# Optimization experiments

Measured on AMD Instinct MI355X. Metric: run time of the kernel, lower is better.

The kernel has to match this reference:

```python
import jax, jax.numpy as jnp
import numpy as np

B, S, E, H, D = 64, 512, 512, 8, 64  # batch, n_steps, embedding_size, head_count, QKV_dim

def setup_inputs() -> dict:
    key = jax.random.key(0)
    ks = jax.random.split(key, 7)
    x = jax.random.normal(ks[0], (B, S, E), dtype=jnp.float32)
    mask = jax.random.randint(ks[1], (B, S), 0, 2).astype(jnp.float32)  # 1 = masked out
    WQ = jax.random.normal(ks[2], (H, E, D), dtype=jnp.float32) * 0.1
    WK = jax.random.normal(ks[3], (H, E, D), dtype=jnp.float32) * 0.1
    WV = jax.random.normal(ks[4], (H, E, D), dtype=jnp.float32) * 0.1
    BE = jax.random.normal(ks[5], (S, E), dtype=jnp.float32) * 0.1
    WO = jax.random.normal(ks[6], (H * D, E), dtype=jnp.float32) * 0.1
    return {"x": x, "mask": mask, "WQ": WQ, "WK": WK, "WV": WV, "BE": BE, "WO": WO}

def reference(x, mask, WQ, WK, WV, BE, WO):
    # add learned positional bias
    h = x + BE  # [B,S,E]
    # per-head projections, vectorized over heads
    Q = jnp.einsum('bse,hed->bhsd', h, WQ)
    K = jnp.einsum('bse,hed->bhsd', h, WK)
    V = jnp.einsum('bse,hed->bhsd', h, WV)
    # NOTE: original scales by sqrt(embedding_size), not sqrt(QKV_dim)
    scores = jnp.einsum('bhsd,bhtd->bhst', Q, K) / np.sqrt(E).astype(np.float32)
    # additive mask trick: mask tiled over query dim, key positions masked where mask==1
    scores = scores - mask[:, None, None, :] * 1e10
    alpha = jax.nn.softmax(scores, axis=-1)  # [B,H,S,S]
    attn = jnp.einsum('bhst,bhtd->bhsd', alpha, V)  # [B,H,S,D]
    # concat heads along feature dim -> [B,S,H*D], then output projection
    attn = jnp.transpose(attn, (0, 2, 1, 3)).reshape(x.shape[0], x.shape[1], -1)
    return attn @ WO  # [B,S,E]
```

## Files before the change

### kernel.cpp

```cpp
#include <hip/hip_runtime.h>
#include <hip/hip_bf16.h>


#define Bn 64
#define Sn 512
#define En 512
#define Hn 8
#define Dn 64

typedef __attribute__((ext_vector_type(8))) short s8v;
typedef __attribute__((ext_vector_type(4))) float f4v;

__device__ __forceinline__ unsigned short f2bf(float f) {
    union { float f; unsigned int u; } v; v.f = f;
    unsigned int u = v.u;
    u += 0x7fffu + ((u >> 16) & 1u);
    return (unsigned short)(u >> 16);
}

__device__ __forceinline__ void async16(const unsigned short* g, unsigned short* l) {
    __builtin_amdgcn_global_load_lds((const __attribute__((address_space(1))) void*)g,
                                     (__attribute__((address_space(3))) void*)l, 16, 0, 0);
}
__device__ __forceinline__ void async4(const float* g, float* l) {
    __builtin_amdgcn_global_load_lds((const __attribute__((address_space(1))) void*)g,
                                     (__attribute__((address_space(3))) void*)l, 4, 0, 0);
}

__global__ __launch_bounds__(256) void prep_all(const float* __restrict__ x,
                                                const float* __restrict__ BE,
                                                const float* __restrict__ WQ,
                                                const float* __restrict__ WK,
                                                const float* __restrict__ WV,
                                                const float* __restrict__ WO,
                                                unsigned short* __restrict__ hbf,
                                                unsigned short* __restrict__ Wqkvt,
                                                unsigned short* __restrict__ WOt) {
    int bid = blockIdx.x;
    if (bid < 16384) {
        int i = (bid * 256 + threadIdx.x) * 4;
        int se = i % (Sn * En);
        float4 a = *(const float4*)(x + i);
        float4 b = *(const float4*)(BE + se);
        ushort4 o;
        o.x = f2bf(a.x + b.x); o.y = f2bf(a.y + b.y);
        o.z = f2bf(a.z + b.z); o.w = f2bf(a.w + b.w);
        *(ushort4*)(hbf + i) = o;
    } else {
        int idx = (bid - 16384) * 256 + threadIdx.x;
        const int NW = 3 * Hn * Dn * En;
        if (idx < NW) {
            int e = idx & 511;
            int d = (idx >> 9) & 63;
            int h = (idx >> 15) & 7;
            int m = idx >> 18;
            const float* W = (m == 0) ? WQ : (m == 1) ? WK : WV;
            Wqkvt[idx] = f2bf(W[(h * En + e) * Dn + d]);
        } else {
            int j = idx - NW;
            int n = j & 511;
            int e = j >> 9;
            WOt[j] = f2bf(WO[n * En + e]);
        }
    }
}

__device__ __forceinline__ void mfma8(const s8v& a0k0, const s8v& a0k1,
                                      const s8v& a1k0, const s8v& a1k1,
                                      f4v* acc0, f4v* acc1,
                                      const s8v (&bq)[4][2], bool sw) {
    if (sw) {
#pragma unroll
        for (int n = 0; n < 4; n++) {
            acc0[n] = __builtin_amdgcn_mfma_f32_16x16x32_bf16(bq[n][0], a0k0, acc0[n], 0, 0, 0);
            acc0[n] = __builtin_amdgcn_mfma_f32_16x16x32_bf16(bq[n][1], a0k1, acc0[n], 0, 0, 0);
            acc1[n] = __builtin_amdgcn_mfma_f32_16x16x32_bf16(bq[n][0], a1k0, acc1[n], 0, 0, 0);
            acc1[n] = __builtin_amdgcn_mfma_f32_16x16x32_bf16(bq[n][1], a1k1, acc1[n], 0, 0, 0);
        }
    } else {
#pragma unroll
        for (int n = 0; n < 4; n++) {
            acc0[n] = __builtin_amdgcn_mfma_f32_16x16x32_bf16(a0k0, bq[n][0], acc0[n], 0, 0, 0);
            acc0[n] = __builtin_amdgcn_mfma_f32_16x16x32_bf16(a0k1, bq[n][1], acc0[n], 0, 0, 0);
            acc1[n] = __builtin_amdgcn_mfma_f32_16x16x32_bf16(a1k0, bq[n][0], acc1[n], 0, 0, 0);
            acc1[n] = __builtin_amdgcn_mfma_f32_16x16x32_bf16(a1k1, bq[n][1], acc1[n], 0, 0, 0);
        }
    }
}

__global__ __launch_bounds__(512, 2) void qkv_gemm(const unsigned short* __restrict__ hbf,
                                                   const unsigned short* __restrict__ Wqkvt,
                                                   unsigned short* __restrict__ Qo,
                                                   unsigned short* __restrict__ Ko,
                                                   unsigned short* __restrict__ Vt) {
    __shared__ __align__(16) unsigned short As[2][16384];
    __shared__ __align__(16) unsigned short Bs[2][16384];

    int lin = blockIdx.y * 6 + blockIdx.x;
    int swz = (lin & 7) * 96 + (lin >> 3);
    int mb = swz / 6, nbv = swz - mb * 6;

    int tid = threadIdx.x;
    int w = tid >> 6, lane = tid & 63, quad = lane >> 4, l16 = lane & 15, l7 = l16 & 7;
    int wr = w >> 2, wcn = w & 3;

    const unsigned short* Ag = hbf + (size_t)mb * 256 * 512;
    const unsigned short* Bg = Wqkvt + (size_t)nbv * 256 * 512;

    int colbase = nbv * 256 + wcn * 64;
    bool swapQK = colbase < 1024;

    int ha = (lane >> 3) & 1;
    int ca = w * 4 + (lane >> 4);
    int aG0 = (ca + 128 * ha) * 512 + ((lane & 7) ^ (ca & 7)) * 8;
    int rb0 = w * 8 + (lane >> 3);
    int bG0 = rb0 * 512 + ((lane & 7) ^ (rb0 & 7)) * 8;

    int arow = 2 * l16 + wr;
    int aseg0 = (quad ^ l7) * 8;
    int aseg1 = ((4 + quad) ^ l7) * 8;

    f4v acc[8][4];
#pragma unroll
    for (int i = 0; i < 8; i++)
#pragma unroll
        for (int n = 0; n < 4; n++) acc[i][n] = (f4v){0.f, 0.f, 0.f, 0.f};
    s8v bq[4][2];

#define STA8(o_, p_, kt_) async16(Ag + aG0 + (p_) * 16384 + (kt_) * 64, &As[o_][(p_) * 4096 + w * 512])
#define STB8(o_, q_, kt_) async16(Bg + bG0 + (q_) * 32768 + (kt_) * 64, &Bs[o_][(q_) * 4096 + w * 512])

#define PHASE8(P, STAGES, GATE)                                                   \
    do {                                                                          \
        if ((P) == 0) {                                                           \
            _Pragma("unroll")                                                     \
            for (int n = 0; n < 4; n++) {                                         \
                int br = (wcn * 64 + n * 16 + l16) * 64;                          \
                bq[n][0] = *(const s8v*)&Bs_s[br + aseg0];                        \
                bq[n][1] = *(const s8v*)&Bs_s[br + aseg1];                        \
            }                                                                     \
        }                                                                         \
        s8v a0k0 = *(const s8v*)&As_s[(((P) * 2 + 0) * 32 + arow) * 64 + aseg0];  \
        s8v a0k1 = *(const s8v*)&As_s[(((P) * 2 + 0) * 32 + arow) * 64 + aseg1];  \
        s8v a1k0 = *(const s8v*)&As_s[(((P) * 2 + 1) * 32 + arow) * 64 + aseg0];  \
        s8v a1k1 = *(const s8v*)&As_s[(((P) * 2 + 1) * 32 + arow) * 64 + aseg1];  \
        STAGES;                                                                   \
        __builtin_amdgcn_s_barrier();                                             \
        asm volatile("s_waitcnt lgkmcnt(0)" ::: "memory");                        \
        __builtin_amdgcn_s_setprio(1);                                            \
        mfma8(a0k0, a0k1, a1k0, a1k1, &acc[(P) * 2][0], &acc[(P) * 2 + 1][0], bq, swapQK); \
        __builtin_amdgcn_s_setprio(0);                                            \
        GATE;                                                                     \
        __builtin_amdgcn_s_barrier();                                             \
    } while (0)

    STB8(0, 0, 0); STB8(0, 1, 0); STB8(0, 2, 0); STB8(0, 3, 0);
    STA8(0, 0, 0); STA8(0, 1, 0); STA8(0, 2, 0); STA8(0, 3, 0);
    asm volatile("s_waitcnt vmcnt(0)" ::: "memory");
    __builtin_amdgcn_s_barrier();

    for (int k = 0; k < 7; k++) {
        int s = k & 1, o = s ^ 1, kt = k + 1;
        const unsigned short* As_s = &As[s][0];
        const unsigned short* Bs_s = &Bs[s][0];
        PHASE8(0, { STB8(o, 0, kt); STB8(o, 1, kt); STA8(o, 0, kt); },
               asm volatile("s_waitcnt vmcnt(6)" ::: "memory"));
        PHASE8(1, { STB8(o, 2, kt); STA8(o, 1, kt); },
               asm volatile("s_waitcnt vmcnt(6)" ::: "memory"));
        PHASE8(2, { STB8(o, 3, kt); STA8(o, 2, kt); },
               asm volatile("s_waitcnt vmcnt(7)" ::: "memory"));
        PHASE8(3, { STA8(o, 3, kt); },
               asm volatile("s_waitcnt vmcnt(2)" ::: "memory"));
    }
    {
        const unsigned short* As_s = &As[1][0];
        const unsigned short* Bs_s = &Bs[1][0];
        PHASE8(0, {}, asm volatile("s_waitcnt vmcnt(3)" ::: "memory"));
        PHASE8(1, {}, asm volatile("s_waitcnt vmcnt(1)" ::: "memory"));
        PHASE8(2, {}, asm volatile("s_waitcnt vmcnt(0)" ::: "memory"));
        PHASE8(3, {}, (void)0);
    }
#undef PHASE8
#undef STA8
#undef STB8

    int mat = colbase >> 9;
    int h = (colbase >> 6) & 7;
    int b_idx = mb >> 1;
    const float qscale = 0.06375873f;

    if (swapQK) {
        unsigned short* op = (mat == 0) ? Qo : Ko;
        float sc = (mat == 0) ? qscale : 1.0f;
#pragma unroll
        for (int mi = 0; mi < 8; mi++)
#pragma unroll
            for (int n = 0; n < 4; n++) {
                int s_ = (mb & 1) * 256 + wr * 128 + mi * 16 + l16;
                int d0 = n * 16 + quad * 4;
                ushort4 pk;
                pk.x = f2bf(acc[mi][n][0] * sc);
                pk.y = f2bf(acc[mi][n][1] * sc);
                pk.z = f2bf(acc[mi][n][2] * sc);
                pk.w = f2bf(acc[mi][n][3] * sc);
                *(ushort4*)&op[(size_t)((b_idx * Hn + h) * Sn + s_) * Dn + d0] = pk;
            }
    } else {
#pragma unroll
        for (int mi = 0; mi < 8; mi++)
#pragma unroll
            for (int n = 0; n < 4; n++) {
                int d = n * 16 + l16;
                int srow = (mb & 1) * 256 + wr * 128 + mi * 16 + quad * 4;
                ushort4 pk;
                pk.x = f2bf(acc[mi][n][0]); pk.y = f2bf(acc[mi][n][1]);
                pk.z = f2bf(acc[mi][n][2]); pk.w = f2bf(acc[mi][n][3]);
                *(ushort4*)&Vt[(size_t)((b_idx * Hn + h) * Dn + d) * Sn + srow] = pk;
            }
    }
}

__global__ __launch_bounds__(512) void attn_kernel(const unsigned short* __restrict__ Q,
                                                   const unsigned short* __restrict__ K,
                                                   const unsigned short* __restrict__ Vt,
                                                   const float* __restrict__ mask,
                                                   unsigned short* __restrict__ attn) {
    int bh = blockIdx.x;
    int h = bh & 7, b = bh >> 3;
    __shared__ __align__(16) unsigned short Kc[64 * 64];
    __shared__ __align__(16) unsigned short Vc[64 * 64];
    __shared__ __align__(16) unsigned short Ps[8][2 * 16 * 64];
    __shared__ float maskv[64];
    int tid = threadIdx.x;
    int w = tid >> 6, lane = tid & 63, quad = lane >> 4, l16 = lane & 15;
    int l7 = l16 & 7;

    const unsigned short* Qg = Q + (size_t)(bh * Sn) * Dn;
    const unsigned short* Kg = K + (size_t)(bh * Sn) * Dn;
    const unsigned short* Vg = Vt + (size_t)(bh * Dn) * Sn;

    s8v aq[4][2];
#pragma unroll
    for (int i = 0; i < 4; i++)
#pragma unroll
        for (int ks = 0; ks < 2; ks++)
            aq[i][ks] = *(const s8v*)&Qg[((w * 4 + i) * 16 + l16) * 64 + ks * 32 + quad * 8];

    f4v acc[4][4];
    float psum[4] = {0.f, 0.f, 0.f, 0.f};
#pragma unroll
    for (int i = 0; i < 4; i++)
#pragma unroll
        for (int n = 0; n < 4; n++) acc[i][n] = (f4v){0.f, 0.f, 0.f, 0.f};

    int srow = w * 8 + (lane >> 3);
    int gseg = ((lane & 7) ^ (srow & 7)) * 8;
    unsigned short* kdst = &Kc[(w * 8) * 64];
    unsigned short* vdst = &Vc[(w * 8) * 64];

    unsigned short* Pw = Ps[w];
    int wbase = l16 * 64 + (quad & 1) * 4;
    const float cM = -1.4426950409e10f;

    for (int kc = 0; kc < 8; kc++) {
        __syncthreads();
        async16(Kg + (kc * 64 + srow) * 64 + gseg, kdst);
        async16(Vg + srow * 512 + kc * 64 + gseg, vdst);
        if (w == 0) async4(mask + b * Sn + kc * 64 + lane, maskv);
        __syncthreads();

#pragma unroll
        for (int p = 0; p < 2; p++) {
#pragma unroll
            for (int n = 0; n < 4; n++) {
                s8v bk0 = *(const s8v*)&Kc[(n * 16 + l16) * 64 + (quad ^ l7) * 8];
                s8v bk1 = *(const s8v*)&Kc[(n * 16 + l16) * 64 + ((4 + quad) ^ l7) * 8];
                float4 mv = *(const float4*)&maskv[n * 16 + quad * 4];
                float m0 = mv.x * cM, m1 = mv.y * cM, m2 = mv.z * cM, m3 = mv.w * cM;
                int wseg = ((n * 2 + (quad >> 1)) ^ l7) * 8;
                f4v sacc[2];
#pragma unroll
                for (int j = 0; j < 2; j++) {
                    int i = p * 2 + j;
                    sacc[j] = __builtin_amdgcn_mfma_f32_16x16x32_bf16(
                                  bk0, aq[i][0], (f4v){0.f, 0.f, 0.f, 0.f}, 0, 0, 0);
                    sacc[j] = __builtin_amdgcn_mfma_f32_16x16x32_bf16(
                                  bk1, aq[i][1], sacc[j], 0, 0, 0);
                }
#pragma unroll
                for (int j = 0; j < 2; j++) {
                    unsigned int u0 = __float_as_uint(__builtin_amdgcn_exp2f(sacc[j][0] + m0));
                    unsigned int u1 = __float_as_uint(__builtin_amdgcn_exp2f(sacc[j][1] + m1));
                    unsigned int u2 = __float_as_uint(__builtin_amdgcn_exp2f(sacc[j][2] + m2));
                    unsigned int u3 = __float_as_uint(__builtin_amdgcn_exp2f(sacc[j][3] + m3));
                    psum[p * 2 + j] += __uint_as_float(u0 & 0xffff0000u) + __uint_as_float(u1 & 0xffff0000u)
                                     + __uint_as_float(u2 & 0xffff0000u) + __uint_as_float(u3 & 0xffff0000u);
                    uint2 pk;
                    pk.x = (u0 >> 16) | (u1 & 0xffff0000u);
                    pk.y = (u2 >> 16) | (u3 & 0xffff0000u);
                    *(uint2*)&Pw[(j << 10) + wbase + wseg] = pk;
                }
            }
#pragma unroll
            for (int ks = 0; ks < 2; ks++) {
                int sw = ((ks * 4 + quad) ^ l7) * 8;
                s8v ap[2];
#pragma unroll
                for (int j = 0; j < 2; j++)
                    ap[j] = *(const s8v*)&Pw[(j << 10) + l16 * 64 + sw];
#pragma unroll
                for (int n = 0; n < 4; n++) {
                    s8v bv = *(const s8v*)&Vc[(n * 16 + l16) * 64 + sw];
#pragma unroll
                    for (int j = 0; j < 2; j++)
                        acc[p * 2 + j][n] = __builtin_amdgcn_mfma_f32_16x16x32_bf16(ap[j], bv, acc[p * 2 + j][n], 0, 0, 0);
                }
            }
        }
    }

#pragma unroll
    for (int i = 0; i < 4; i++) {
        float s = psum[i];
        s += __shfl_xor(s, 16, 64);
        s += __shfl_xor(s, 32, 64);
        float inv[4];
#pragma unroll
        for (int r = 0; r < 4; r++)
            inv[r] = 1.0f / __shfl(s, quad * 4 + r, 64);
#pragma unroll
        for (int n = 0; n < 4; n++)
#pragma unroll
            for (int r = 0; r < 4; r++) {
                int query = (w * 4 + i) * 16 + quad * 4 + r;
                int col = h * 64 + n * 16 + l16;
                attn[(size_t)(b * Sn + query) * (Hn * Dn) + col] = f2bf(acc[i][n][r] * inv[r]);
            }
    }
}

__global__ __launch_bounds__(512, 2) void outproj(const unsigned short* __restrict__ attn,
                                                  const unsigned short* __restrict__ WOt,
                                                  float* __restrict__ out) {
    __shared__ __align__(16) unsigned short As[2][16384];
    __shared__ __align__(16) unsigned short Bs[2][16384];

    int lin = blockIdx.y * 2 + blockIdx.x;
    int swz = (lin & 7) * 32 + (lin >> 3);
    int mb = swz >> 1, nbv = swz & 1;

    int tid = threadIdx.x;
    int w = tid >> 6, lane = tid & 63, quad = lane >> 4, l16 = lane & 15, l7 = l16 & 7;
    int wr = w >> 2, wcn = w & 3;

    const unsigned short* Ag = attn + (size_t)mb * 256 * 512;
    const unsigned short* Bg = WOt + (size_t)nbv * 256 * 512;

    int ha = (lane >> 3) & 1;
    int ca = w * 4 + (lane >> 4);
    int aG0 = (ca + 128 * ha) * 512 + ((lane & 7) ^ (ca & 7)) * 8;
    int rb0 = w * 8 + (lane >> 3);
    int bG0 = rb0 * 512 + ((lane & 7) ^ (rb0 & 7)) * 8;

    int arow = 2 * l16 + wr;
    int aseg0 = (quad ^ l7) * 8;
    int aseg1 = ((4 + quad) ^ l7) * 8;

    f4v acc[8][4];
#pragma unroll
    for (int i = 0; i < 8; i++)
#pragma unroll
        for (int n = 0; n < 4; n++) acc[i][n] = (f4v){0.f, 0.f, 0.f, 0.f};
    s8v bq[4][2];

#define STA8(o_, p_, kt_) async16(Ag + aG0 + (p_) * 16384 + (kt_) * 64, &As[o_][(p_) * 4096 + w * 512])
#define STB8(o_, q_, kt_) async16(Bg + bG0 + (q_) * 32768 + (kt_) * 64, &Bs[o_][(q_) * 4096 + w * 512])

#define PHASE8(P, STAGES, GATE)                                                   \
    do {                                                                          \
        if ((P) == 0) {                                                           \
            _Pragma("unroll")                                                     \
            for (int n = 0; n < 4; n++) {                                         \
                int br = (wcn * 64 + n * 16 + l16) * 64;                          \
                bq[n][0] = *(const s8v*)&Bs_s[br + aseg0];                        \
                bq[n][1] = *(const s8v*)&Bs_s[br + aseg1];                        \
            }                                                                     \
        }                                                                         \
        s8v a0k0 = *(const s8v*)&As_s[(((P) * 2 + 0) * 32 + arow) * 64 + aseg0];  \
        s8v a0k1 = *(const s8v*)&As_s[(((P) * 2 + 0) * 32 + arow) * 64 + aseg1];  \
        s8v a1k0 = *(const s8v*)&As_s[(((P) * 2 + 1) * 32 + arow) * 64 + aseg0];  \
        s8v a1k1 = *(const s8v*)&As_s[(((P) * 2 + 1) * 32 + arow) * 64 + aseg1];  \
        STAGES;                                                                   \
        __builtin_amdgcn_s_barrier();                                             \
        asm volatile("s_waitcnt lgkmcnt(0)" ::: "memory");                        \
        __builtin_amdgcn_s_setprio(1);                                            \
        mfma8(a0k0, a0k1, a1k0, a1k1, &acc[(P) * 2][0], &acc[(P) * 2 + 1][0], bq, true); \
        __builtin_amdgcn_s_setprio(0);                                            \
        GATE;                                                                     \
        __builtin_amdgcn_s_barrier();                                             \
    } while (0)

    STB8(0, 0, 0); STB8(0, 1, 0); STB8(0, 2, 0); STB8(0, 3, 0);
    STA8(0, 0, 0); STA8(0, 1, 0); STA8(0, 2, 0); STA8(0, 3, 0);
    asm volatile("s_waitcnt vmcnt(0)" ::: "memory");
    __builtin_amdgcn_s_barrier();

    for (int k = 0; k < 7; k++) {
        int s = k & 1, o = s ^ 1, kt = k + 1;
        const unsigned short* As_s = &As[s][0];
        const unsigned short* Bs_s = &Bs[s][0];
        PHASE8(0, { STB8(o, 0, kt); STB8(o, 1, kt); STA8(o, 0, kt); },
               asm volatile("s_waitcnt vmcnt(6)" ::: "memory"));
        PHASE8(1, { STB8(o, 2, kt); STA8(o, 1, kt); },
               asm volatile("s_waitcnt vmcnt(6)" ::: "memory"));
        PHASE8(2, { STB8(o, 3, kt); STA8(o, 2, kt); },
               asm volatile("s_waitcnt vmcnt(7)" ::: "memory"));
        PHASE8(3, { STA8(o, 3, kt); },
               asm volatile("s_waitcnt vmcnt(2)" ::: "memory"));
    }
    {
        const unsigned short* As_s = &As[1][0];
        const unsigned short* Bs_s = &Bs[1][0];
        PHASE8(0, {}, asm volatile("s_waitcnt vmcnt(3)" ::: "memory"));
        PHASE8(1, {}, asm volatile("s_waitcnt vmcnt(1)" ::: "memory"));
        PHASE8(2, {}, asm volatile("s_waitcnt vmcnt(0)" ::: "memory"));
        PHASE8(3, {}, (void)0);
    }
#undef PHASE8
#undef STA8
#undef STB8

#pragma unroll
    for (int mi = 0; mi < 8; mi++)
#pragma unroll
        for (int n = 0; n < 4; n++) {
            int row = mb * 256 + wr * 128 + mi * 16 + l16;
            int col = nbv * 256 + wcn * 64 + n * 16 + quad * 4;
            float4 o;
            o.x = acc[mi][n][0]; o.y = acc[mi][n][1];
            o.z = acc[mi][n][2]; o.w = acc[mi][n][3];
            *(float4*)&out[(size_t)row * 512 + col] = o;
        }
}

extern "C" void kernel_launch(void* const* d_in, const int* in_sizes, int n_in,
                              void* d_out, int out_size, void* d_ws, size_t ws_size,
                              hipStream_t stream) {
    const float* x    = (const float*)d_in[0];
    const float* mask = (const float*)d_in[1];
    const float* WQ   = (const float*)d_in[2];
    const float* WK   = (const float*)d_in[3];
    const float* WV   = (const float*)d_in[4];
    const float* BE   = (const float*)d_in[5];
    const float* WO   = (const float*)d_in[6];
    float* out = (float*)d_out;

    char* ws = (char*)d_ws;
    unsigned short* hbf   = (unsigned short*)(ws);
    unsigned short* Wqkvt = (unsigned short*)(ws + 33554432);
    unsigned short* WOt   = (unsigned short*)(ws + 35127296);
    unsigned short* Qp    = (unsigned short*)(ws + 35651584);
    unsigned short* Kp    = (unsigned short*)(ws + 69206016);
    unsigned short* Vtp   = (unsigned short*)(ws + 102760448);
    unsigned short* attnp = (unsigned short*)(ws + 136314880);

    prep_all<<<20480, 256, 0, stream>>>(x, BE, WQ, WK, WV, WO, hbf, Wqkvt, WOt);
    qkv_gemm<<<dim3(6, 128), 512, 0, stream>>>(hbf, Wqkvt, Qp, Kp, Vtp);
    attn_kernel<<<512, 512, 0, stream>>>(Qp, Kp, Vtp, mask, attnp);
    outproj<<<dim3(2, 128), 512, 0, stream>>>(attnp, WOt, out);
}
```

Measured before the change: 287.3 us.

## Double-buffer K/V tiles, preload mask, and transpose PV MFMA for vector stores

Double-buffers the K and V LDS tiles so the next chunk's async loads overlap compute on the current chunk, which cuts two barriers per iteration down to one. The whole mask row is preloaded once. The PV MFMA operands are swapped so each lane holds a query row's contiguous D values, allowing 8-byte packed bf16 stores and removing the cross-lane shuffles for the normalizer. It adds LDS use, which may lower occupancy, and whether the single barrier per iteration is enough ordering depends on the async LDS load semantics.

```diff
diff --git a/kernel.cpp b/kernel.cpp
--- a/kernel.cpp
+++ b/kernel.cpp
@@ -227,10 +227,10 @@
                                                    unsigned short* __restrict__ attn) {
     int bh = blockIdx.x;
     int h = bh & 7, b = bh >> 3;
-    __shared__ __align__(16) unsigned short Kc[64 * 64];
-    __shared__ __align__(16) unsigned short Vc[64 * 64];
+    __shared__ __align__(16) unsigned short Kc[2][64 * 64];
+    __shared__ __align__(16) unsigned short Vc[2][64 * 64];
     __shared__ __align__(16) unsigned short Ps[8][2 * 16 * 64];
-    __shared__ float maskv[64];
+    __shared__ float maskv[512];
     int tid = threadIdx.x;
     int w = tid >> 6, lane = tid & 63, quad = lane >> 4, l16 = lane & 15;
     int l7 = l16 & 7;
@@ -255,27 +255,31 @@
 
     int srow = w * 8 + (lane >> 3);
     int gseg = ((lane & 7) ^ (srow & 7)) * 8;
-    unsigned short* kdst = &Kc[(w * 8) * 64];
-    unsigned short* vdst = &Vc[(w * 8) * 64];
+    int kldsoff = (w * 8) * 64;
 
     unsigned short* Pw = Ps[w];
     int wbase = l16 * 64 + (quad & 1) * 4;
     const float cM = -1.4426950409e10f;
 
+    async16(Kg + srow * 64 + gseg, &Kc[0][kldsoff]);
+    async16(Vg + srow * 512 + gseg, &Vc[0][kldsoff]);
+    async4(mask + b * Sn + w * 64 + lane, &maskv[w * 64]);
+    __syncthreads();
+
     for (int kc = 0; kc < 8; kc++) {
-        __syncthreads();
-        async16(Kg + (kc * 64 + srow) * 64 + gseg, kdst);
-        async16(Vg + srow * 512 + kc * 64 + gseg, vdst);
-        if (w == 0) async4(mask + b * Sn + kc * 64 + lane, maskv);
-        __syncthreads();
+        int cur = kc & 1, nxt = cur ^ 1;
+        if (kc < 7) {
+            async16(Kg + ((kc + 1) * 64 + srow) * 64 + gseg, &Kc[nxt][kldsoff]);
+            async16(Vg + srow * 512 + (kc + 1) * 64 + gseg, &Vc[nxt][kldsoff]);
+        }
 
 #pragma unroll
         for (int p = 0; p < 2; p++) {
 #pragma unroll
             for (int n = 0; n < 4; n++) {
-                s8v bk0 = *(const s8v*)&Kc[(n * 16 + l16) * 64 + (quad ^ l7) * 8];
-                s8v bk1 = *(const s8v*)&Kc[(n * 16 + l16) * 64 + ((4 + quad) ^ l7) * 8];
-                float4 mv = *(const float4*)&maskv[n * 16 + quad * 4];
+                s8v bk0 = *(const s8v*)&Kc[cur][(n * 16 + l16) * 64 + (quad ^ l7) * 8];
+                s8v bk1 = *(const s8v*)&Kc[cur][(n * 16 + l16) * 64 + ((4 + quad) ^ l7) * 8];
+                float4 mv = *(const float4*)&maskv[kc * 64 + n * 16 + quad * 4];
                 float m0 = mv.x * cM, m1 = mv.y * cM, m2 = mv.z * cM, m3 = mv.w * cM;
                 int wseg = ((n * 2 + (quad >> 1)) ^ l7) * 8;
                 f4v sacc[2];
@@ -310,13 +314,14 @@
                     ap[j] = *(const s8v*)&Pw[(j << 10) + l16 * 64 + sw];
 #pragma unroll
                 for (int n = 0; n < 4; n++) {
-                    s8v bv = *(const s8v*)&Vc[(n * 16 + l16) * 64 + sw];
+                    s8v bv = *(const s8v*)&Vc[cur][(n * 16 + l16) * 64 + sw];
 #pragma unroll
                     for (int j = 0; j < 2; j++)
-                        acc[p * 2 + j][n] = __builtin_amdgcn_mfma_f32_16x16x32_bf16(ap[j], bv, acc[p * 2 + j][n], 0, 0, 0);
+                        acc[p * 2 + j][n] = __builtin_amdgcn_mfma_f32_16x16x32_bf16(bv, ap[j], acc[p * 2 + j][n], 0, 0, 0);
                 }
             }
         }
+        __syncthreads();
     }
 
 #pragma unroll
@@ -324,18 +329,18 @@
         float s = psum[i];
         s += __shfl_xor(s, 16, 64);
         s += __shfl_xor(s, 32, 64);
-        float inv[4];
-#pragma unroll
-        for (int r = 0; r < 4; r++)
-            inv[r] = 1.0f / __shfl(s, quad * 4 + r, 64);
-#pragma unroll
-        for (int n = 0; n < 4; n++)
-#pragma unroll
-            for (int r = 0; r < 4; r++) {
-                int query = (w * 4 + i) * 16 + quad * 4 + r;
-                int col = h * 64 + n * 16 + l16;
-                attn[(size_t)(b * Sn + query) * (Hn * Dn) + col] = f2bf(acc[i][n][r] * inv[r]);
-            }
+        float inv = 1.0f / s;
+        int query = (w * 4 + i) * 16 + l16;
+#pragma unroll
+        for (int n = 0; n < 4; n++) {
+            int d0 = n * 16 + quad * 4;
+            ushort4 pk;
+            pk.x = f2bf(acc[i][n][0] * inv);
+            pk.y = f2bf(acc[i][n][1] * inv);
+            pk.z = f2bf(acc[i][n][2] * inv);
+            pk.w = f2bf(acc[i][n][3] * inv);
+            *(ushort4*)&attn[(size_t)(b * Sn + query) * (Hn * Dn) + h * 64 + d0] = pk;
+        }
     }
 }
 
```

Result: slower. 294.2 us (+2.4%).
